# Performance work log

Measured on AMD Instinct MI355X. Metric: run time of the kernel, lower is better.

Reference implementation:

```python
import jax, jax.numpy as jnp
import numpy as np

VOCAB = 32000
FEAT = 1024
B, T = 16, 256


def setup_inputs() -> dict:
    key = jax.random.key(0)
    ks = jax.random.split(key, 12)
    s_in = 1.0 / np.sqrt(FEAT)
    inp = {
        "x": jax.random.randint(ks[0], (B, T), 0, VOCAB),
        "h0": jnp.zeros((2, B, FEAT), jnp.float32),
        "emb": jax.random.normal(ks[1], (VOCAB, FEAT), jnp.float32) * 0.02,
        "W_ih0": jax.random.uniform(ks[2], (3 * FEAT, FEAT), jnp.float32, -s_in, s_in),
        "W_hh0": jax.random.uniform(ks[3], (3 * FEAT, FEAT), jnp.float32, -s_in, s_in),
        "b_ih0": jax.random.uniform(ks[4], (3 * FEAT,), jnp.float32, -s_in, s_in),
        "b_hh0": jax.random.uniform(ks[5], (3 * FEAT,), jnp.float32, -s_in, s_in),
        "W_ih1": jax.random.uniform(ks[6], (3 * FEAT, FEAT), jnp.float32, -s_in, s_in),
        "W_hh1": jax.random.uniform(ks[7], (3 * FEAT, FEAT), jnp.float32, -s_in, s_in),
        "b_ih1": jax.random.uniform(ks[8], (3 * FEAT,), jnp.float32, -s_in, s_in),
        "b_hh1": jax.random.uniform(ks[9], (3 * FEAT,), jnp.float32, -s_in, s_in),
        "dec_b": jnp.zeros((VOCAB,), jnp.float32),
    }
    return inp


def _gru_layer(xs, h0, W_ih, W_hh, b_ih, b_hh):
    # xs: [T, B, H_in]; h0: [B, H]. PyTorch gate order: r, z, n.
    x_proj = jnp.einsum('tbi,gi->tbg', xs, W_ih) + b_ih  # [T, B, 3H]

    def step(h, xp):
        hp = h @ W_hh.T + b_hh  # [B, 3H]
        xr, xz, xn = jnp.split(xp, 3, axis=-1)
        hr, hz, hn = jnp.split(hp, 3, axis=-1)
        r = jax.nn.sigmoid(xr + hr)
        z = jax.nn.sigmoid(xz + hz)
        n = jnp.tanh(xn + r * hn)
        h_new = (1.0 - z) * n + z * h
        return h_new, h_new

    h_last, ys = jax.lax.scan(step, h0, x_proj)
    return ys, h_last


def reference(x, h0, emb, W_ih0, W_hh0, b_ih0, b_hh0, W_ih1, W_hh1, b_ih1, b_hh1, dec_b):
    xs = emb[x]  # [B, T, H]
    xs = jnp.transpose(xs, (1, 0, 2))  # time-major [T, B, H]
    ys0, h_last0 = _gru_layer(xs, h0[0], W_ih0, W_hh0, b_ih0, b_hh0)
    ys1, h_last1 = _gru_layer(ys0, h0[1], W_ih1, W_hh1, b_ih1, b_hh1)
    out = jnp.transpose(ys1, (1, 0, 2))  # [B, T, H]
    logits = jnp.einsum('bth,vh->btv', out, emb) + dec_b  # tied decoder
    hidden = jnp.stack([h_last0, h_last1], axis=0)  # [2, B, H]
    return logits, hidden
```

## Files before the change

kernel.cpp:

```cpp
#include <hip/hip_runtime.h>
#include <math.h>

#define FEAT 1024
#define NB 16
#define NT 256
#define VOCAB 32000
#define G3 3072
#define NWG 256
#define FLAG_STRIDE 32
#define NGRP 8
#define GSZ 32

#define BK 32
#define LDH 40

typedef float f4 __attribute__((ext_vector_type(4)));
typedef float f32x4 __attribute__((ext_vector_type(4)));
typedef _Float16 half4v __attribute__((ext_vector_type(4)));
typedef _Float16 half8v __attribute__((ext_vector_type(8)));

__global__ __launch_bounds__(256) void gather_kernel(const int* __restrict__ x,
                                                     const float* __restrict__ emb,
                                                     float* __restrict__ xs) {
    int row = blockIdx.x;
    int t = row >> 4;
    int b = row & 15;
    int tok = x[b * NT + t];
    const float4* src = (const float4*)(emb + (size_t)tok * FEAT);
    float4* dst = (float4*)(xs + (size_t)row * FEAT);
    dst[threadIdx.x] = src[threadIdx.x];
}

__global__ __launch_bounds__(256, 2) void gemm_split16(
        const float* __restrict__ A, const float* __restrict__ Bm,
        const float* __restrict__ bias, float* __restrict__ C,
        int M, int N, int K, int GM, int perm) {
    __shared__ _Float16 AhS[128 * LDH];
    __shared__ _Float16 AlS[128 * LDH];
    __shared__ _Float16 BhS[128 * LDH];
    __shared__ _Float16 BlS[128 * LDH];

    int nNt = N >> 7;
    int perGroup = GM * nNt;
    int g = blockIdx.x / perGroup;
    int rix = blockIdx.x % perGroup;
    int n_t = rix / GM;
    int m_t = g * GM + (rix % GM);

    int tid = threadIdx.x;
    int srow = tid >> 1;
    int shf = tid & 1;

    const float* aptr = A + (size_t)(m_t * 128 + srow) * K + shf * 16;
    const float* bptr = Bm + (size_t)(n_t * 128 + srow) * K + shf * 16;

    int wid = tid >> 6;
    int wr = wid >> 1, wc = wid & 1;
    int lane = tid & 63;
    int fr = lane & 15;
    int ke = lane >> 4;

    f32x4 acc[4][4];
#pragma unroll
    for (int i = 0; i < 4; i++)
#pragma unroll
        for (int j = 0; j < 4; j++) acc[i][j] = (f32x4){0.f, 0.f, 0.f, 0.f};

    float4 a4[4], b4[4];
#pragma unroll
    for (int q = 0; q < 4; q++) {
        a4[q] = *(const float4*)(aptr + q * 4);
        b4[q] = *(const float4*)(bptr + q * 4);
    }

    for (int k0 = 0; k0 < K; k0 += BK) {
        __syncthreads();
#pragma unroll
        for (int q = 0; q < 4; q++) {
            half4v hh, hl;
            hh.x = (_Float16)a4[q].x; hl.x = (_Float16)(a4[q].x - (float)hh.x);
            hh.y = (_Float16)a4[q].y; hl.y = (_Float16)(a4[q].y - (float)hh.y);
            hh.z = (_Float16)a4[q].z; hl.z = (_Float16)(a4[q].z - (float)hh.z);
            hh.w = (_Float16)a4[q].w; hl.w = (_Float16)(a4[q].w - (float)hh.w);
            int o = srow * LDH + shf * 16 + q * 4;
            *(half4v*)&AhS[o] = hh;
            *(half4v*)&AlS[o] = hl;
            half4v gh, gl;
            gh.x = (_Float16)b4[q].x; gl.x = (_Float16)(b4[q].x - (float)gh.x);
            gh.y = (_Float16)b4[q].y; gl.y = (_Float16)(b4[q].y - (float)gh.y);
            gh.z = (_Float16)b4[q].z; gl.z = (_Float16)(b4[q].z - (float)gh.z);
            gh.w = (_Float16)b4[q].w; gl.w = (_Float16)(b4[q].w - (float)gh.w);
            *(half4v*)&BhS[o] = gh;
            *(half4v*)&BlS[o] = gl;
        }
        __syncthreads();

        if (k0 + BK < K) {
#pragma unroll
            for (int q = 0; q < 4; q++) {
                a4[q] = *(const float4*)(aptr + k0 + BK + q * 4);
                b4[q] = *(const float4*)(bptr + k0 + BK + q * 4);
            }
        }

        half8v ah[4], al[4], bh[4], bl[4];
#pragma unroll
        for (int i = 0; i < 4; i++) {
            int ao = (wr * 64 + i * 16 + fr) * LDH + ke * 8;
            ah[i] = *(const half8v*)&AhS[ao];
            al[i] = *(const half8v*)&AlS[ao];
            int bo = (wc * 64 + i * 16 + fr) * LDH + ke * 8;
            bh[i] = *(const half8v*)&BhS[bo];
            bl[i] = *(const half8v*)&BlS[bo];
        }
#pragma unroll
        for (int i = 0; i < 4; i++)
#pragma unroll
            for (int j = 0; j < 4; j++) {
                acc[i][j] = __builtin_amdgcn_mfma_f32_16x16x32_f16(ah[i], bh[j], acc[i][j], 0, 0, 0);
                acc[i][j] = __builtin_amdgcn_mfma_f32_16x16x32_f16(ah[i], bl[j], acc[i][j], 0, 0, 0);
                acc[i][j] = __builtin_amdgcn_mfma_f32_16x16x32_f16(al[i], bh[j], acc[i][j], 0, 0, 0);
            }
    }

#pragma unroll
    for (int j = 0; j < 4; j++) {
        int col = n_t * 128 + wc * 64 + j * 16 + fr;
        float bv = bias[col];
#pragma unroll
        for (int i = 0; i < 4; i++) {
#pragma unroll
            for (int v = 0; v < 4; v++) {
                int mrow = m_t * 128 + wr * 64 + i * 16 + 4 * ke + v;
                int orow = perm ? (((mrow & 15) << 8) | (mrow >> 4)) : mrow;
                C[(size_t)orow * N + col] = acc[i][j][v] + bv;
            }
        }
    }
}

__device__ __forceinline__ void store_f32_sc(float* p, float v) {
    asm volatile("global_store_dword %0, %1, off sc0 sc1" :: "v"(p), "v"(v) : "memory");
}

__global__ __launch_bounds__(256, 1) void gru_scan(const float* __restrict__ xp,
                                                   const float* __restrict__ Whh,
                                                   const float* __restrict__ bhh,
                                                   const float* __restrict__ h0src,
                                                   float* __restrict__ ys,
                                                   float* __restrict__ hid,
                                                   unsigned* __restrict__ flags,
                                                   unsigned* __restrict__ gflags,
                                                   unsigned gen_base) {
    __shared__ float w_lds[12 * 1028];
    __shared__ float red[192 * 65];
    __shared__ float sum_lds[192];
    __shared__ float bhh_lds[12];

    int wg = blockIdx.x;
    int j0 = wg * 4;
    int tid = threadIdx.x;

    for (int rr = 0; rr < 12; rr++) {
        int gate = rr >> 2, jloc = rr & 3;
        int grow = gate * FEAT + j0 + jloc;
        float4 v = ((const float4*)(Whh + (size_t)grow * FEAT))[tid];
        *(float4*)(w_lds + rr * 1028 + tid * 4) = v;
    }
    if (tid < 12) {
        int gate = tid >> 2, jloc = tid & 3;
        bhh_lds[tid] = bhh[gate * FEAT + j0 + jloc];
    }
    __syncthreads();

    int bg = tid >> 6;
    int kc = tid & 63;
    int pb = tid >> 2, pjl = tid & 3, pj = j0 + pjl;

    float xr = 0.f, xz = 0.f, xnv = 0.f, hreg = 0.f;
    if (tid < 64) {
        const float* xpr = xp + (size_t)(0 * NB + pb) * G3;
        xr = xpr[pj]; xz = xpr[FEAT + pj]; xnv = xpr[2 * FEAT + pj];
        hreg = h0src[pb * FEAT + pj];
    }

    for (int t = 0; t < NT; t++) {
        const float* hc = (t == 0) ? h0src : (ys + (size_t)(t - 1) * NB * FEAT);

        f4 h4[16];
#pragma unroll
        for (int bi = 0; bi < 4; bi++) {
            const float* hp = hc + (size_t)(bg * 4 + bi) * FEAT + kc * 4;
#pragma unroll
            for (int q = 0; q < 4; q++)
                h4[bi * 4 + q] = *(const f4*)(hp + q * 256);
        }

        float part[48];
#pragma unroll
        for (int i = 0; i < 48; i++) part[i] = 0.f;
#pragma unroll
        for (int q = 0; q < 4; q++) {
            int kof = q * 256 + kc * 4;
#pragma unroll
            for (int rr = 0; rr < 12; rr++) {
                f4 w = *(const f4*)&w_lds[rr * 1028 + kof];
#pragma unroll
                for (int bi = 0; bi < 4; bi++) {
                    part[rr * 4 + bi] = fmaf(h4[bi * 4 + q].x, w.x, part[rr * 4 + bi]);
                    part[rr * 4 + bi] = fmaf(h4[bi * 4 + q].y, w.y, part[rr * 4 + bi]);
                    part[rr * 4 + bi] = fmaf(h4[bi * 4 + q].z, w.z, part[rr * 4 + bi]);
                    part[rr * 4 + bi] = fmaf(h4[bi * 4 + q].w, w.w, part[rr * 4 + bi]);
                }
            }
        }
#pragma unroll
        for (int rr = 0; rr < 12; rr++)
#pragma unroll
            for (int bi = 0; bi < 4; bi++)
                red[(rr * 16 + bg * 4 + bi) * 65 + kc] = part[rr * 4 + bi];
        __syncthreads();

        if (tid < 192) {
            float s = 0.f;
#pragma unroll
            for (int q = 0; q < 64; q++) s += red[tid * 65 + q];
            sum_lds[tid] = s;
        }
        __syncthreads();

        if (tid < 64) {
            float dr = sum_lds[pjl * 16 + pb] + bhh_lds[pjl];
            float dz = sum_lds[(4 + pjl) * 16 + pb] + bhh_lds[4 + pjl];
            float dn = sum_lds[(8 + pjl) * 16 + pb] + bhh_lds[8 + pjl];
            float r = 1.f / (1.f + expf(-(xr + dr)));
            float z = 1.f / (1.f + expf(-(xz + dz)));
            float n = tanhf(xnv + r * dn);
            float hv = (1.f - z) * n + z * hreg;
            hreg = hv;
            store_f32_sc(ys + (size_t)(t * NB + pb) * FEAT + pj, hv);
            if (t == NT - 1) hid[pb * FEAT + pj] = hv;
        }

        unsigned expected = gen_base + t + 1;
        __syncthreads();
        if (tid == 0) {
            asm volatile("s_waitcnt vmcnt(0)\n\t"
                         "global_store_dword %0, %1, off sc0 sc1"
                         :: "v"(&flags[wg * FLAG_STRIDE]), "v"(expected) : "memory");
        }
        if (tid < 64) {
            int tn = (t + 1 < NT) ? t + 1 : t;
            const float* xpr = xp + (size_t)(tn * NB + pb) * G3;
            xr = xpr[pj]; xz = xpr[FEAT + pj]; xnv = xpr[2 * FEAT + pj];
        }
        if (wg < NGRP) {
            if (tid < GSZ) {
                const unsigned* fp = flags + (wg * GSZ + tid) * FLAG_STRIDE;
                unsigned v; int spins = 0;
                while (true) {
                    asm volatile("global_load_dword %0, %1, off sc0 sc1\n\t"
                                 "s_waitcnt vmcnt(0)"
                                 : "=&v"(v) : "v"(fp) : "memory");
                    if (v >= expected) break;
                    if (++spins > (1 << 20)) break;
                    __builtin_amdgcn_s_sleep(1);
                }
            }
            if (tid == 0) {
                asm volatile("global_store_dword %0, %1, off sc0 sc1"
                             :: "v"(&gflags[wg * FLAG_STRIDE]), "v"(expected) : "memory");
            }
        }
        if (tid < NGRP) {
            const unsigned* gp = gflags + tid * FLAG_STRIDE;
            unsigned v; int spins = 0;
            while (true) {
                asm volatile("global_load_dword %0, %1, off sc0 sc1\n\t"
                             "s_waitcnt vmcnt(0)"
                             : "=&v"(v) : "v"(gp) : "memory");
                if (v >= expected) break;
                if (++spins > (1 << 20)) break;
                __builtin_amdgcn_s_sleep(1);
            }
        }
        __builtin_amdgcn_sched_barrier(0);
        __syncthreads();
    }
}

extern "C" void kernel_launch(void* const* d_in, const int* in_sizes, int n_in,
                              void* d_out, int out_size, void* d_ws, size_t ws_size,
                              hipStream_t stream) {
    const int*   x     = (const int*)d_in[0];
    const float* h0    = (const float*)d_in[1];
    const float* emb   = (const float*)d_in[2];
    const float* W_ih0 = (const float*)d_in[3];
    const float* W_hh0 = (const float*)d_in[4];
    const float* b_ih0 = (const float*)d_in[5];
    const float* b_hh0 = (const float*)d_in[6];
    const float* W_ih1 = (const float*)d_in[7];
    const float* W_hh1 = (const float*)d_in[8];
    const float* b_ih1 = (const float*)d_in[9];
    const float* b_hh1 = (const float*)d_in[10];
    const float* dec_b = (const float*)d_in[11];

    float* out = (float*)d_out;
    float* hid_out = out + (size_t)NB * NT * VOCAB;

    float* ws  = (float*)d_ws;
    float* xp  = ws;
    float* xs  = xp + (size_t)4096 * 3072;
    float* ys0 = xs + (size_t)4096 * 1024;
    float* ha  = ys0 + (size_t)4096 * 1024;
    float* hb  = ha + NB * FEAT;
    unsigned* flags  = (unsigned*)(hb + NB * FEAT);
    unsigned* gflags = flags + NWG * FLAG_STRIDE;
    float* ys1 = xs;

    hipMemsetAsync((void*)flags, 0,
                   (NWG + NGRP) * FLAG_STRIDE * sizeof(unsigned), stream);

    gather_kernel<<<dim3(NT * NB), dim3(256), 0, stream>>>(x, emb, xs);

    gemm_split16<<<dim3((4096 / 128) * (G3 / 128)), dim3(256), 0, stream>>>(
        xs, W_ih0, b_ih0, xp, 4096, G3, FEAT, 8, 0);

    gru_scan<<<dim3(NWG), dim3(256), 0, stream>>>(
        xp, W_hh0, b_hh0, h0, ys0, hid_out, flags, gflags, 0u);

    gemm_split16<<<dim3((4096 / 128) * (G3 / 128)), dim3(256), 0, stream>>>(
        ys0, W_ih1, b_ih1, xp, 4096, G3, FEAT, 8, 0);

    gru_scan<<<dim3(NWG), dim3(256), 0, stream>>>(
        xp, W_hh1, b_hh1, h0 + NB * FEAT, ys1, hid_out + NB * FEAT,
        flags, gflags, (unsigned)NT);

    gemm_split16<<<dim3((4096 / 128) * (VOCAB / 128)), dim3(256), 0, stream>>>(
        ys1, emb, dec_b, out, 4096, VOCAB, FEAT, 8, 1);
}
```

Measured before the change: 3.619 ms.

## Fuse both GRU layers into one wavefront-pipelined persistent scan kernel

Replaces the two sequential GRU scan launches and the intermediate layer-1 input-projection GEMM with one persistent kernel. At step s it computes layer 0 at time s and layer 1 at time s-1, so there are 257 grid barriers instead of 512. Layer 1 computes its W_ih1 projection inline by reading W_ih1 from global memory (L2) each step, while both W_hh matrices stay in LDS. It also halves the LDS reduction with a lane-pair shuffle and rotates the barrier-aggregator group each step. The cost is more per-step work and register pressure (64 extra partials), plus repeated global loads of W_ih1 on the critical path.

After: 4.786 ms. 32.3% more time.

```diff
diff --git a/kernel.cpp b/kernel.cpp
--- a/kernel.cpp
+++ b/kernel.cpp
@@ -143,19 +143,19 @@
     asm volatile("global_store_dword %0, %1, off sc0 sc1" :: "v"(p), "v"(v) : "memory");
 }
 
-__global__ __launch_bounds__(256, 1) void gru_scan(const float* __restrict__ xp,
-                                                   const float* __restrict__ Whh,
-                                                   const float* __restrict__ bhh,
-                                                   const float* __restrict__ h0src,
-                                                   float* __restrict__ ys,
-                                                   float* __restrict__ hid,
-                                                   unsigned* __restrict__ flags,
-                                                   unsigned* __restrict__ gflags,
-                                                   unsigned gen_base) {
-    __shared__ float w_lds[12 * 1028];
-    __shared__ float red[192 * 65];
-    __shared__ float sum_lds[192];
-    __shared__ float bhh_lds[12];
+__global__ __launch_bounds__(256, 1) void gru_fused(
+        const float* __restrict__ xp0,
+        const float* __restrict__ Whh0, const float* __restrict__ bhh0,
+        const float* __restrict__ Wih1, const float* __restrict__ bih1,
+        const float* __restrict__ Whh1, const float* __restrict__ bhh1,
+        const float* __restrict__ h0all,
+        float* __restrict__ ys0, float* __restrict__ ys1,
+        float* __restrict__ hid,
+        unsigned* __restrict__ flags, unsigned* __restrict__ gflags) {
+    __shared__ float wl0[12 * 1024];
+    __shared__ float wl1[12 * 1024];
+    __shared__ float red[256 * 33];
+    __shared__ float sumA[256];
 
     int wg = blockIdx.x;
     int j0 = wg * 4;
@@ -164,12 +164,10 @@
     for (int rr = 0; rr < 12; rr++) {
         int gate = rr >> 2, jloc = rr & 3;
         int grow = gate * FEAT + j0 + jloc;
-        float4 v = ((const float4*)(Whh + (size_t)grow * FEAT))[tid];
-        *(float4*)(w_lds + rr * 1028 + tid * 4) = v;
-    }
-    if (tid < 12) {
-        int gate = tid >> 2, jloc = tid & 3;
-        bhh_lds[tid] = bhh[gate * FEAT + j0 + jloc];
+        *(float4*)(wl0 + rr * 1024 + tid * 4) =
+            ((const float4*)(Whh0 + (size_t)grow * FEAT))[tid];
+        *(float4*)(wl1 + rr * 1024 + tid * 4) =
+            ((const float4*)(Whh1 + (size_t)grow * FEAT))[tid];
     }
     __syncthreads();
 
@@ -177,115 +175,222 @@
     int kc = tid & 63;
     int pb = tid >> 2, pjl = tid & 3, pj = j0 + pjl;
 
-    float xr = 0.f, xz = 0.f, xnv = 0.f, hreg = 0.f;
+    float xr = 0.f, xz = 0.f, xnv = 0.f;
+    float hreg0 = 0.f, hreg1 = 0.f;
+    float b0r = 0.f, b0z = 0.f, b0n = 0.f;
+    float bi1r = 0.f, bi1z = 0.f, bi1n = 0.f;
+    float bh1r = 0.f, bh1z = 0.f, bh1n = 0.f;
     if (tid < 64) {
-        const float* xpr = xp + (size_t)(0 * NB + pb) * G3;
+        const float* xpr = xp0 + (size_t)(0 * NB + pb) * G3;
         xr = xpr[pj]; xz = xpr[FEAT + pj]; xnv = xpr[2 * FEAT + pj];
-        hreg = h0src[pb * FEAT + pj];
-    }
-
-    for (int t = 0; t < NT; t++) {
-        const float* hc = (t == 0) ? h0src : (ys + (size_t)(t - 1) * NB * FEAT);
-
-        f4 h4[16];
+        hreg0 = h0all[pb * FEAT + pj];
+        hreg1 = h0all[NB * FEAT + pb * FEAT + pj];
+        b0r = bhh0[pj]; b0z = bhh0[FEAT + pj]; b0n = bhh0[2 * FEAT + pj];
+        bi1r = bih1[pj]; bi1z = bih1[FEAT + pj]; bi1n = bih1[2 * FEAT + pj];
+        bh1r = bhh1[pj]; bh1z = bhh1[FEAT + pj]; bh1n = bhh1[2 * FEAT + pj];
+    }
+
+    const float* wih_r = Wih1 + (size_t)(0 * FEAT) * FEAT;
+    const float* wih_z = Wih1 + (size_t)(1 * FEAT) * FEAT;
+    const float* wih_n = Wih1 + (size_t)(2 * FEAT) * FEAT;
+
+    for (int s = 0; s <= NT; s++) {
+        const float* v01src = (s == 0) ? h0all
+                                       : (ys0 + (size_t)(s - 1) * NB * FEAT);
+        f4 v01[16];
 #pragma unroll
         for (int bi = 0; bi < 4; bi++) {
-            const float* hp = hc + (size_t)(bg * 4 + bi) * FEAT + kc * 4;
-#pragma unroll
-            for (int q = 0; q < 4; q++)
-                h4[bi * 4 + q] = *(const f4*)(hp + q * 256);
-        }
-
-        float part[48];
-#pragma unroll
-        for (int i = 0; i < 48; i++) part[i] = 0.f;
-#pragma unroll
-        for (int q = 0; q < 4; q++) {
-            int kof = q * 256 + kc * 4;
-#pragma unroll
-            for (int rr = 0; rr < 12; rr++) {
-                f4 w = *(const f4*)&w_lds[rr * 1028 + kof];
-#pragma unroll
-                for (int bi = 0; bi < 4; bi++) {
-                    part[rr * 4 + bi] = fmaf(h4[bi * 4 + q].x, w.x, part[rr * 4 + bi]);
-                    part[rr * 4 + bi] = fmaf(h4[bi * 4 + q].y, w.y, part[rr * 4 + bi]);
-                    part[rr * 4 + bi] = fmaf(h4[bi * 4 + q].z, w.z, part[rr * 4 + bi]);
-                    part[rr * 4 + bi] = fmaf(h4[bi * 4 + q].w, w.w, part[rr * 4 + bi]);
+            const float* p = v01src + (size_t)(bg * 4 + bi) * FEAT + kc * 4;
+#pragma unroll
+            for (int q = 0; q < 4; q++) v01[bi * 4 + q] = *(const f4*)(p + q * 256);
+        }
+        f4 v1[16];
+        if (s >= 1) {
+            const float* v1src = (s == 1) ? (h0all + NB * FEAT)
+                                          : (ys1 + (size_t)(s - 2) * NB * FEAT);
+#pragma unroll
+            for (int bi = 0; bi < 4; bi++) {
+                const float* p = v1src + (size_t)(bg * 4 + bi) * FEAT + kc * 4;
+#pragma unroll
+                for (int q = 0; q < 4; q++) v1[bi * 4 + q] = *(const f4*)(p + q * 256);
+            }
+        }
+
+        if (s < NT) {
+            float part[48];
+#pragma unroll
+            for (int i = 0; i < 48; i++) part[i] = 0.f;
+#pragma unroll
+            for (int q = 0; q < 4; q++) {
+                int kof = q * 256 + kc * 4;
+#pragma unroll
+                for (int rr = 0; rr < 12; rr++) {
+                    f4 w = *(const f4*)&wl0[rr * 1024 + kof];
+#pragma unroll
+                    for (int bi = 0; bi < 4; bi++) {
+                        f4 h = v01[bi * 4 + q];
+                        float p = part[rr * 4 + bi];
+                        p = fmaf(h.x, w.x, p); p = fmaf(h.y, w.y, p);
+                        p = fmaf(h.z, w.z, p); p = fmaf(h.w, w.w, p);
+                        part[rr * 4 + bi] = p;
+                    }
                 }
             }
-        }
-#pragma unroll
-        for (int rr = 0; rr < 12; rr++)
-#pragma unroll
-            for (int bi = 0; bi < 4; bi++)
-                red[(rr * 16 + bg * 4 + bi) * 65 + kc] = part[rr * 4 + bi];
-        __syncthreads();
-
-        if (tid < 192) {
-            float s = 0.f;
-#pragma unroll
-            for (int q = 0; q < 64; q++) s += red[tid * 65 + q];
-            sum_lds[tid] = s;
-        }
-        __syncthreads();
-
-        if (tid < 64) {
-            float dr = sum_lds[pjl * 16 + pb] + bhh_lds[pjl];
-            float dz = sum_lds[(4 + pjl) * 16 + pb] + bhh_lds[4 + pjl];
-            float dn = sum_lds[(8 + pjl) * 16 + pb] + bhh_lds[8 + pjl];
+#pragma unroll
+            for (int i = 0; i < 48; i++) part[i] += __shfl_xor(part[i], 1);
+            if ((kc & 1) == 0) {
+#pragma unroll
+                for (int rr = 0; rr < 12; rr++)
+#pragma unroll
+                    for (int bi = 0; bi < 4; bi++)
+                        red[(rr * 16 + bg * 4 + bi) * 33 + (kc >> 1)] =
+                            part[rr * 4 + bi];
+            }
+        }
+        __syncthreads();
+        if (s < NT && tid < 192) {
+            float t0 = 0.f;
+#pragma unroll
+            for (int c = 0; c < 32; c++) t0 += red[tid * 33 + c];
+            sumA[tid] = t0;
+        }
+        __syncthreads();
+        if (s < NT && tid < 64) {
+            float dr = sumA[pjl * 16 + pb] + b0r;
+            float dz = sumA[(4 + pjl) * 16 + pb] + b0z;
+            float dn = sumA[(8 + pjl) * 16 + pb] + b0n;
             float r = 1.f / (1.f + expf(-(xr + dr)));
             float z = 1.f / (1.f + expf(-(xz + dz)));
             float n = tanhf(xnv + r * dn);
-            float hv = (1.f - z) * n + z * hreg;
-            hreg = hv;
-            store_f32_sc(ys + (size_t)(t * NB + pb) * FEAT + pj, hv);
-            if (t == NT - 1) hid[pb * FEAT + pj] = hv;
-        }
-
-        unsigned expected = gen_base + t + 1;
-        __syncthreads();
-        if (tid == 0) {
-            asm volatile("s_waitcnt vmcnt(0)\n\t"
-                         "global_store_dword %0, %1, off sc0 sc1"
-                         :: "v"(&flags[wg * FLAG_STRIDE]), "v"(expected) : "memory");
-        }
-        if (tid < 64) {
-            int tn = (t + 1 < NT) ? t + 1 : t;
-            const float* xpr = xp + (size_t)(tn * NB + pb) * G3;
-            xr = xpr[pj]; xz = xpr[FEAT + pj]; xnv = xpr[2 * FEAT + pj];
-        }
-        if (wg < NGRP) {
-            if (tid < GSZ) {
-                const unsigned* fp = flags + (wg * GSZ + tid) * FLAG_STRIDE;
+            float hv = (1.f - z) * n + z * hreg0;
+            hreg0 = hv;
+            store_f32_sc(ys0 + (size_t)(s * NB + pb) * FEAT + pj, hv);
+            if (s == NT - 1) hid[pb * FEAT + pj] = hv;
+        }
+
+        if (s >= 1) {
+            float p1[64];
+#pragma unroll
+            for (int i = 0; i < 64; i++) p1[i] = 0.f;
+#pragma unroll
+            for (int q = 0; q < 4; q++) {
+                int kof = q * 256 + kc * 4;
+#pragma unroll
+                for (int jl = 0; jl < 4; jl++) {
+                    f4 wir = *(const f4*)(wih_r + (size_t)(j0 + jl) * FEAT + kof);
+                    f4 wiz = *(const f4*)(wih_z + (size_t)(j0 + jl) * FEAT + kof);
+                    f4 win = *(const f4*)(wih_n + (size_t)(j0 + jl) * FEAT + kof);
+                    f4 whr = *(const f4*)&wl1[(0 + jl) * 1024 + kof];
+                    f4 whz = *(const f4*)&wl1[(4 + jl) * 1024 + kof];
+                    f4 whn = *(const f4*)&wl1[(8 + jl) * 1024 + kof];
+#pragma unroll
+                    for (int bi = 0; bi < 4; bi++) {
+                        f4 a = v01[bi * 4 + q];
+                        f4 b = v1[bi * 4 + q];
+                        float pr = p1[(jl) * 4 + bi];
+                        pr = fmaf(a.x, wir.x, pr); pr = fmaf(a.y, wir.y, pr);
+                        pr = fmaf(a.z, wir.z, pr); pr = fmaf(a.w, wir.w, pr);
+                        pr = fmaf(b.x, whr.x, pr); pr = fmaf(b.y, whr.y, pr);
+                        pr = fmaf(b.z, whr.z, pr); pr = fmaf(b.w, whr.w, pr);
+                        p1[(jl) * 4 + bi] = pr;
+                        float pz = p1[(4 + jl) * 4 + bi];
+                        pz = fmaf(a.x, wiz.x, pz); pz = fmaf(a.y, wiz.y, pz);
+                        pz = fmaf(a.z, wiz.z, pz); pz = fmaf(a.w, wiz.w, pz);
+                        pz = fmaf(b.x, whz.x, pz); pz = fmaf(b.y, whz.y, pz);
+                        pz = fmaf(b.z, whz.z, pz); pz = fmaf(b.w, whz.w, pz);
+                        p1[(4 + jl) * 4 + bi] = pz;
+                        float pn = p1[(8 + jl) * 4 + bi];
+                        pn = fmaf(a.x, win.x, pn); pn = fmaf(a.y, win.y, pn);
+                        pn = fmaf(a.z, win.z, pn); pn = fmaf(a.w, win.w, pn);
+                        p1[(8 + jl) * 4 + bi] = pn;
+                        float ph = p1[(12 + jl) * 4 + bi];
+                        ph = fmaf(b.x, whn.x, ph); ph = fmaf(b.y, whn.y, ph);
+                        ph = fmaf(b.z, whn.z, ph); ph = fmaf(b.w, whn.w, ph);
+                        p1[(12 + jl) * 4 + bi] = ph;
+                    }
+                }
+            }
+#pragma unroll
+            for (int i = 0; i < 64; i++) p1[i] += __shfl_xor(p1[i], 1);
+            if ((kc & 1) == 0) {
+#pragma unroll
+                for (int sl = 0; sl < 16; sl++)
+#pragma unroll
+                    for (int bi = 0; bi < 4; bi++)
+                        red[(sl * 16 + bg * 4 + bi) * 33 + (kc >> 1)] =
+                            p1[sl * 4 + bi];
+            }
+        }
+        __syncthreads();
+        if (s >= 1) {
+            float t1 = 0.f;
+#pragma unroll
+            for (int c = 0; c < 32; c++) t1 += red[tid * 33 + c];
+            sumA[tid] = t1;
+        }
+        __syncthreads();
+        if (s >= 1 && tid < 64) {
+            float mr = sumA[(0 + pjl) * 16 + pb] + bi1r + bh1r;
+            float mz = sumA[(4 + pjl) * 16 + pb] + bi1z + bh1z;
+            float in = sumA[(8 + pjl) * 16 + pb] + bi1n;
+            float hn = sumA[(12 + pjl) * 16 + pb] + bh1n;
+            float r = 1.f / (1.f + expf(-mr));
+            float z = 1.f / (1.f + expf(-mz));
+            float n = tanhf(in + r * hn);
+            float hv = (1.f - z) * n + z * hreg1;
+            hreg1 = hv;
+            store_f32_sc(ys1 + (size_t)((s - 1) * NB + pb) * FEAT + pj, hv);
+            if (s - 1 == NT - 1) hid[NB * FEAT + pb * FEAT + pj] = hv;
+        }
+
+        if (s < NT) {
+            unsigned expected = (unsigned)(s + 1);
+            __syncthreads();
+            if (tid == 0) {
+                asm volatile("s_waitcnt vmcnt(0)\n\t"
+                             "global_store_dword %0, %1, off sc0 sc1"
+                             :: "v"(&flags[wg * FLAG_STRIDE]), "v"(expected) : "memory");
+            }
+            if (tid < 64) {
+                int tn = (s + 1 < NT) ? s + 1 : NT - 1;
+                const float* xpr = xp0 + (size_t)(tn * NB + pb) * G3;
+                xr = xpr[pj]; xz = xpr[FEAT + pj]; xnv = xpr[2 * FEAT + pj];
+            }
+            int lid = wg - ((s * NGRP) & (NWG - 1));
+            if (lid < 0) lid += NWG;
+            if (lid < NGRP) {
+                if (tid < GSZ) {
+                    const unsigned* fp = flags + (lid * GSZ + tid) * FLAG_STRIDE;
+                    unsigned v; int spins = 0;
+                    while (true) {
+                        asm volatile("global_load_dword %0, %1, off sc0 sc1\n\t"
+                                     "s_waitcnt vmcnt(0)"
+                                     : "=&v"(v) : "v"(fp) : "memory");
+                        if (v >= expected) break;
+                        if (++spins > (1 << 20)) break;
+                        __builtin_amdgcn_s_sleep(1);
+                    }
+                }
+                if (tid == 0) {
+                    asm volatile("global_store_dword %0, %1, off sc0 sc1"
+                                 :: "v"(&gflags[lid * FLAG_STRIDE]), "v"(expected) : "memory");
+                }
+            }
+            if (tid < NGRP) {
+                const unsigned* gp = gflags + tid * FLAG_STRIDE;
                 unsigned v; int spins = 0;
                 while (true) {
                     asm volatile("global_load_dword %0, %1, off sc0 sc1\n\t"
                                  "s_waitcnt vmcnt(0)"
-                                 : "=&v"(v) : "v"(fp) : "memory");
+                                 : "=&v"(v) : "v"(gp) : "memory");
                     if (v >= expected) break;
                     if (++spins > (1 << 20)) break;
                     __builtin_amdgcn_s_sleep(1);
                 }
             }
-            if (tid == 0) {
-                asm volatile("global_store_dword %0, %1, off sc0 sc1"
-                             :: "v"(&gflags[wg * FLAG_STRIDE]), "v"(expected) : "memory");
-            }
-        }
-        if (tid < NGRP) {
-            const unsigned* gp = gflags + tid * FLAG_STRIDE;
-            unsigned v; int spins = 0;
-            while (true) {
-                asm volatile("global_load_dword %0, %1, off sc0 sc1\n\t"
-                             "s_waitcnt vmcnt(0)"
-                             : "=&v"(v) : "v"(gp) : "memory");
-                if (v >= expected) break;
-                if (++spins > (1 << 20)) break;
-                __builtin_amdgcn_s_sleep(1);
-            }
-        }
-        __builtin_amdgcn_sched_barrier(0);
-        __syncthreads();
+            __builtin_amdgcn_sched_barrier(0);
+            __syncthreads();
+        }
     }
 }
 
@@ -312,9 +417,8 @@
     float* xp  = ws;
     float* xs  = xp + (size_t)4096 * 3072;
     float* ys0 = xs + (size_t)4096 * 1024;
-    float* ha  = ys0 + (size_t)4096 * 1024;
-    float* hb  = ha + NB * FEAT;
-    unsigned* flags  = (unsigned*)(hb + NB * FEAT);
+    float* pad = ys0 + (size_t)4096 * 1024;
+    unsigned* flags  = (unsigned*)(pad + 2 * NB * FEAT);
     unsigned* gflags = flags + NWG * FLAG_STRIDE;
     float* ys1 = xs;
 
@@ -326,15 +430,9 @@
     gemm_split16<<<dim3((4096 / 128) * (G3 / 128)), dim3(256), 0, stream>>>(
         xs, W_ih0, b_ih0, xp, 4096, G3, FEAT, 8, 0);
 
-    gru_scan<<<dim3(NWG), dim3(256), 0, stream>>>(
-        xp, W_hh0, b_hh0, h0, ys0, hid_out, flags, gflags, 0u);
-
-    gemm_split16<<<dim3((4096 / 128) * (G3 / 128)), dim3(256), 0, stream>>>(
-        ys0, W_ih1, b_ih1, xp, 4096, G3, FEAT, 8, 0);
-
-    gru_scan<<<dim3(NWG), dim3(256), 0, stream>>>(
-        xp, W_hh1, b_hh1, h0 + NB * FEAT, ys1, hid_out + NB * FEAT,
-        flags, gflags, (unsigned)NT);
+    gru_fused<<<dim3(NWG), dim3(256), 0, stream>>>(
+        xp, W_hh0, b_hh0, W_ih1, b_ih1, W_hh1, b_hh1, h0,
+        ys0, ys1, hid_out, flags, gflags);
 
     gemm_split16<<<dim3((4096 / 128) * (VOCAB / 128)), dim3(256), 0, stream>>>(
         ys1, emb, dec_b, out, 4096, VOCAB, FEAT, 8, 1);
```

## Fuse GRU scan with downstream GEMM in flag-gated persistent kernels

Applied to the files above, without the earlier changes.

Each GRU layer scan is merged into one launch with the GEMM that consumes its output: the layer-1 input projection in the first launch, the tied decoder in the second. Extra GEMM blocks poll the scan's group flags and start on a 128-row tile as soon as the 8 timesteps it covers are complete, so the GEMM overlaps the latency-bound recurrence instead of running after it. The scan also pre-reduces partial sums with a lane shuffle, halving the LDS reduction buffer so shared memory fits two blocks per CU. The risks are that spinning GEMM blocks take CU slots and bandwidth from the scan, that correctness depends on all scan blocks being co-resident, and that layer-1 GEMM overwrites xp while the scan still reads later rows.

After: 3.625 ms. About the same (+0.2%).

```diff
diff --git a/kernel.cpp b/kernel.cpp
--- a/kernel.cpp
+++ b/kernel.cpp
@@ -13,6 +13,7 @@
 
 #define BK 32
 #define LDH 40
+#define SMEM_BYTES 75584
 
 typedef float f4 __attribute__((ext_vector_type(4)));
 typedef float f32x4 __attribute__((ext_vector_type(4)));
@@ -31,21 +32,34 @@
     dst[threadIdx.x] = src[threadIdx.x];
 }
 
-__global__ __launch_bounds__(256, 2) void gemm_split16(
+__device__ __forceinline__ void store_f32_sc(float* p, float v) {
+    asm volatile("global_store_dword %0, %1, off sc0 sc1" :: "v"(p), "v"(v) : "memory");
+}
+__device__ __forceinline__ void bar_arrive(unsigned* flag, unsigned expected) {
+    asm volatile("s_waitcnt vmcnt(0)\n\t"
+                 "global_store_dword %0, %1, off sc0 sc1"
+                 :: "v"(flag), "v"(expected) : "memory");
+}
+__device__ __forceinline__ void bar_poll(const unsigned* p, unsigned expected) {
+    unsigned v; int spins = 0;
+    while (true) {
+        asm volatile("global_load_dword %0, %1, off sc0 sc1\n\t"
+                     "s_waitcnt vmcnt(0)"
+                     : "=&v"(v) : "v"(p) : "memory");
+        if (v >= expected) break;
+        if (++spins > (1 << 20)) break;
+        __builtin_amdgcn_s_sleep(1);
+    }
+}
+
+__device__ __forceinline__ void gemm_tile(char* smemraw,
         const float* __restrict__ A, const float* __restrict__ Bm,
         const float* __restrict__ bias, float* __restrict__ C,
-        int M, int N, int K, int GM, int perm) {
-    __shared__ _Float16 AhS[128 * LDH];
-    __shared__ _Float16 AlS[128 * LDH];
-    __shared__ _Float16 BhS[128 * LDH];
-    __shared__ _Float16 BlS[128 * LDH];
-
-    int nNt = N >> 7;
-    int perGroup = GM * nNt;
-    int g = blockIdx.x / perGroup;
-    int rix = blockIdx.x % perGroup;
-    int n_t = rix / GM;
-    int m_t = g * GM + (rix % GM);
+        int N, int K, int m_t, int n_t, int perm) {
+    _Float16* AhS = (_Float16*)smemraw;
+    _Float16* AlS = AhS + 128 * LDH;
+    _Float16* BhS = AlS + 128 * LDH;
+    _Float16* BlS = BhS + 128 * LDH;
 
     int tid = threadIdx.x;
     int srow = tid >> 1;
@@ -139,23 +153,29 @@
     }
 }
 
-__device__ __forceinline__ void store_f32_sc(float* p, float v) {
-    asm volatile("global_store_dword %0, %1, off sc0 sc1" :: "v"(p), "v"(v) : "memory");
-}
-
-__global__ __launch_bounds__(256, 1) void gru_scan(const float* __restrict__ xp,
-                                                   const float* __restrict__ Whh,
-                                                   const float* __restrict__ bhh,
-                                                   const float* __restrict__ h0src,
-                                                   float* __restrict__ ys,
-                                                   float* __restrict__ hid,
-                                                   unsigned* __restrict__ flags,
-                                                   unsigned* __restrict__ gflags,
-                                                   unsigned gen_base) {
-    __shared__ float w_lds[12 * 1028];
-    __shared__ float red[192 * 65];
-    __shared__ float sum_lds[192];
-    __shared__ float bhh_lds[12];
+__global__ __launch_bounds__(256, 2) void gemm_split16(
+        const float* __restrict__ A, const float* __restrict__ Bm,
+        const float* __restrict__ bias, float* __restrict__ C,
+        int N, int K, int GM, int perm) {
+    __shared__ __align__(16) char smem[4 * 128 * LDH * 2];
+    int nNt = N >> 7;
+    int perGroup = GM * nNt;
+    int g = blockIdx.x / perGroup;
+    int rix = blockIdx.x % perGroup;
+    int n_t = rix / GM;
+    int m_t = g * GM + (rix % GM);
+    gemm_tile(smem, A, Bm, bias, C, N, K, m_t, n_t, perm);
+}
+
+__device__ __forceinline__ void scan_layer(char* smemraw,
+        const float* __restrict__ xp, const float* __restrict__ Whh,
+        const float* __restrict__ bhh, const float* __restrict__ h0src,
+        float* __restrict__ ys, float* __restrict__ hid,
+        unsigned* __restrict__ flags, unsigned* __restrict__ gflags) {
+    float* w_lds   = (float*)smemraw;
+    float* red     = w_lds + 12 * 1024;
+    float* sums    = red + 192 * 33;
+    float* bhh_lds = sums + 256;
 
     int wg = blockIdx.x;
     int j0 = wg * 4;
@@ -165,7 +185,7 @@
         int gate = rr >> 2, jloc = rr & 3;
         int grow = gate * FEAT + j0 + jloc;
         float4 v = ((const float4*)(Whh + (size_t)grow * FEAT))[tid];
-        *(float4*)(w_lds + rr * 1028 + tid * 4) = v;
+        *(float4*)(w_lds + rr * 1024 + tid * 4) = v;
     }
     if (tid < 12) {
         int gate = tid >> 2, jloc = tid & 3;
@@ -204,35 +224,40 @@
             int kof = q * 256 + kc * 4;
 #pragma unroll
             for (int rr = 0; rr < 12; rr++) {
-                f4 w = *(const f4*)&w_lds[rr * 1028 + kof];
+                f4 w = *(const f4*)&w_lds[rr * 1024 + kof];
 #pragma unroll
                 for (int bi = 0; bi < 4; bi++) {
-                    part[rr * 4 + bi] = fmaf(h4[bi * 4 + q].x, w.x, part[rr * 4 + bi]);
-                    part[rr * 4 + bi] = fmaf(h4[bi * 4 + q].y, w.y, part[rr * 4 + bi]);
-                    part[rr * 4 + bi] = fmaf(h4[bi * 4 + q].z, w.z, part[rr * 4 + bi]);
-                    part[rr * 4 + bi] = fmaf(h4[bi * 4 + q].w, w.w, part[rr * 4 + bi]);
+                    f4 h = h4[bi * 4 + q];
+                    float p = part[rr * 4 + bi];
+                    p = fmaf(h.x, w.x, p); p = fmaf(h.y, w.y, p);
+                    p = fmaf(h.z, w.z, p); p = fmaf(h.w, w.w, p);
+                    part[rr * 4 + bi] = p;
                 }
             }
         }
 #pragma unroll
-        for (int rr = 0; rr < 12; rr++)
-#pragma unroll
-            for (int bi = 0; bi < 4; bi++)
-                red[(rr * 16 + bg * 4 + bi) * 65 + kc] = part[rr * 4 + bi];
+        for (int i = 0; i < 48; i++) part[i] += __shfl_xor(part[i], 1);
+        if ((kc & 1) == 0) {
+#pragma unroll
+            for (int rr = 0; rr < 12; rr++)
+#pragma unroll
+                for (int bi = 0; bi < 4; bi++)
+                    red[(rr * 16 + bg * 4 + bi) * 33 + (kc >> 1)] = part[rr * 4 + bi];
+        }
         __syncthreads();
 
         if (tid < 192) {
             float s = 0.f;
 #pragma unroll
-            for (int q = 0; q < 64; q++) s += red[tid * 65 + q];
-            sum_lds[tid] = s;
+            for (int c = 0; c < 32; c++) s += red[tid * 33 + c];
+            sums[tid] = s;
         }
         __syncthreads();
 
         if (tid < 64) {
-            float dr = sum_lds[pjl * 16 + pb] + bhh_lds[pjl];
-            float dz = sum_lds[(4 + pjl) * 16 + pb] + bhh_lds[4 + pjl];
-            float dn = sum_lds[(8 + pjl) * 16 + pb] + bhh_lds[8 + pjl];
+            float dr = sums[pjl * 16 + pb] + bhh_lds[pjl];
+            float dz = sums[(4 + pjl) * 16 + pb] + bhh_lds[4 + pjl];
+            float dn = sums[(8 + pjl) * 16 + pb] + bhh_lds[8 + pjl];
             float r = 1.f / (1.f + expf(-(xr + dr)));
             float z = 1.f / (1.f + expf(-(xz + dz)));
             float n = tanhf(xnv + r * dn);
@@ -242,50 +267,70 @@
             if (t == NT - 1) hid[pb * FEAT + pj] = hv;
         }
 
-        unsigned expected = gen_base + t + 1;
-        __syncthreads();
-        if (tid == 0) {
-            asm volatile("s_waitcnt vmcnt(0)\n\t"
-                         "global_store_dword %0, %1, off sc0 sc1"
-                         :: "v"(&flags[wg * FLAG_STRIDE]), "v"(expected) : "memory");
-        }
+        unsigned expected = (unsigned)(t + 1);
+        __syncthreads();
+        if (tid == 0) bar_arrive(&flags[wg * FLAG_STRIDE], expected);
         if (tid < 64) {
             int tn = (t + 1 < NT) ? t + 1 : t;
             const float* xpr = xp + (size_t)(tn * NB + pb) * G3;
             xr = xpr[pj]; xz = xpr[FEAT + pj]; xnv = xpr[2 * FEAT + pj];
         }
         if (wg < NGRP) {
-            if (tid < GSZ) {
-                const unsigned* fp = flags + (wg * GSZ + tid) * FLAG_STRIDE;
-                unsigned v; int spins = 0;
-                while (true) {
-                    asm volatile("global_load_dword %0, %1, off sc0 sc1\n\t"
-                                 "s_waitcnt vmcnt(0)"
-                                 : "=&v"(v) : "v"(fp) : "memory");
-                    if (v >= expected) break;
-                    if (++spins > (1 << 20)) break;
-                    __builtin_amdgcn_s_sleep(1);
-                }
-            }
+            if (tid < GSZ) bar_poll(flags + (wg * GSZ + tid) * FLAG_STRIDE, expected);
             if (tid == 0) {
                 asm volatile("global_store_dword %0, %1, off sc0 sc1"
                              :: "v"(&gflags[wg * FLAG_STRIDE]), "v"(expected) : "memory");
             }
         }
-        if (tid < NGRP) {
-            const unsigned* gp = gflags + tid * FLAG_STRIDE;
-            unsigned v; int spins = 0;
-            while (true) {
-                asm volatile("global_load_dword %0, %1, off sc0 sc1\n\t"
-                             "s_waitcnt vmcnt(0)"
-                             : "=&v"(v) : "v"(gp) : "memory");
-                if (v >= expected) break;
-                if (++spins > (1 << 20)) break;
-                __builtin_amdgcn_s_sleep(1);
-            }
-        }
+        if (tid < NGRP) bar_poll(gflags + tid * FLAG_STRIDE, expected);
         __builtin_amdgcn_sched_barrier(0);
         __syncthreads();
+    }
+}
+
+__global__ __launch_bounds__(256, 2) void phase1(
+        const float* __restrict__ xp, const float* __restrict__ Whh0,
+        const float* __restrict__ bhh0, const float* __restrict__ h0,
+        float* __restrict__ ys0, float* __restrict__ hid,
+        unsigned* __restrict__ flags0, unsigned* __restrict__ gflags0,
+        const float* __restrict__ Wih1, const float* __restrict__ bih1,
+        float* __restrict__ xpw) {
+    __shared__ __align__(16) char smem[SMEM_BYTES];
+    if (blockIdx.x < NWG) {
+        scan_layer(smem, xp, Whh0, bhh0, h0, ys0, hid, flags0, gflags0);
+    } else {
+        int bid = blockIdx.x - NWG;
+        int perGroup = 8 * (G3 >> 7);
+        int g = bid / perGroup, rix = bid % perGroup;
+        int n_t = rix / 8, m_t = g * 8 + (rix % 8);
+        unsigned gate = (unsigned)((m_t + 1) * 8);
+        if (threadIdx.x < NGRP) bar_poll(gflags0 + threadIdx.x * FLAG_STRIDE, gate);
+        __builtin_amdgcn_sched_barrier(0);
+        __syncthreads();
+        gemm_tile(smem, ys0, Wih1, bih1, xpw, G3, FEAT, m_t, n_t, 0);
+    }
+}
+
+__global__ __launch_bounds__(256, 2) void phase2(
+        const float* __restrict__ xp, const float* __restrict__ Whh1,
+        const float* __restrict__ bhh1, const float* __restrict__ h0b,
+        float* __restrict__ ys1, float* __restrict__ hid1,
+        unsigned* __restrict__ flags1, unsigned* __restrict__ gflags1,
+        const float* __restrict__ emb, const float* __restrict__ dec_b,
+        float* __restrict__ out) {
+    __shared__ __align__(16) char smem[SMEM_BYTES];
+    if (blockIdx.x < NWG) {
+        scan_layer(smem, xp, Whh1, bhh1, h0b, ys1, hid1, flags1, gflags1);
+    } else {
+        int bid = blockIdx.x - NWG;
+        int perGroup = 8 * (VOCAB >> 7);
+        int g = bid / perGroup, rix = bid % perGroup;
+        int n_t = rix / 8, m_t = g * 8 + (rix % 8);
+        unsigned gate = (unsigned)((m_t + 1) * 8);
+        if (threadIdx.x < NGRP) bar_poll(gflags1 + threadIdx.x * FLAG_STRIDE, gate);
+        __builtin_amdgcn_sched_barrier(0);
+        __syncthreads();
+        gemm_tile(smem, ys1, emb, dec_b, out, VOCAB, FEAT, m_t, n_t, 1);
     }
 }
 
@@ -312,30 +357,25 @@
     float* xp  = ws;
     float* xs  = xp + (size_t)4096 * 3072;
     float* ys0 = xs + (size_t)4096 * 1024;
-    float* ha  = ys0 + (size_t)4096 * 1024;
-    float* hb  = ha + NB * FEAT;
-    unsigned* flags  = (unsigned*)(hb + NB * FEAT);
-    unsigned* gflags = flags + NWG * FLAG_STRIDE;
+    float* pad = ys0 + (size_t)4096 * 1024;
+    unsigned* flags0  = (unsigned*)(pad + 2 * NB * FEAT);
+    unsigned* gflags0 = flags0 + NWG * FLAG_STRIDE;
+    unsigned* flags1  = gflags0 + NGRP * FLAG_STRIDE;
+    unsigned* gflags1 = flags1 + NWG * FLAG_STRIDE;
     float* ys1 = xs;
 
-    hipMemsetAsync((void*)flags, 0,
-                   (NWG + NGRP) * FLAG_STRIDE * sizeof(unsigned), stream);
+    hipMemsetAsync((void*)flags0, 0,
+                   (2 * NWG + 2 * NGRP) * FLAG_STRIDE * sizeof(unsigned), stream);
 
     gather_kernel<<<dim3(NT * NB), dim3(256), 0, stream>>>(x, emb, xs);
 
     gemm_split16<<<dim3((4096 / 128) * (G3 / 128)), dim3(256), 0, stream>>>(
-        xs, W_ih0, b_ih0, xp, 4096, G3, FEAT, 8, 0);
-
-    gru_scan<<<dim3(NWG), dim3(256), 0, stream>>>(
-        xp, W_hh0, b_hh0, h0, ys0, hid_out, flags, gflags, 0u);
-
-    gemm_split16<<<dim3((4096 / 128) * (G3 / 128)), dim3(256), 0, stream>>>(
-        ys0, W_ih1, b_ih1, xp, 4096, G3, FEAT, 8, 0);
-
-    gru_scan<<<dim3(NWG), dim3(256), 0, stream>>>(
+        xs, W_ih0, b_ih0, xp, G3, FEAT, 8, 0);
+
+    phase1<<<dim3(NWG + (4096 / 128) * (G3 / 128)), dim3(256), 0, stream>>>(
+        xp, W_hh0, b_hh0, h0, ys0, hid_out, flags0, gflags0, W_ih1, b_ih1, xp);
+
+    phase2<<<dim3(NWG + (4096 / 128) * (VOCAB / 128)), dim3(256), 0, stream>>>(
         xp, W_hh1, b_hh1, h0 + NB * FEAT, ys1, hid_out + NB * FEAT,
-        flags, gflags, (unsigned)NT);
-
-    gemm_split16<<<dim3((4096 / 128) * (VOCAB / 128)), dim3(256), 0, stream>>>(
-        ys1, emb, dec_b, out, 4096, VOCAB, FEAT, 8, 1);
-}
+        flags1, gflags1, emb, dec_b, out);
+}
```
